# Kernel optimization log

Measured on AMD Instinct MI355X. Metric: run time of the kernel, lower is better.

## Reference

```python
import jax, jax.numpy as jnp
import numpy as np

T, IN_DIM, HID, OUT = 32768, 500, 300, 100


def setup_inputs() -> dict:
    key = jax.random.key(0)
    ks = jax.random.split(key, 12)
    s_in = 1.0 / np.sqrt(HID)
    inp = {
        'input_seq': jax.random.normal(ks[0], (T, IN_DIM), jnp.float32),
        'W_ih0': jax.random.uniform(ks[1], (HID, IN_DIM), jnp.float32, -s_in, s_in),
        'W_hh0': jax.random.uniform(ks[2], (HID, HID), jnp.float32, -s_in, s_in),
        'b_ih0': jax.random.uniform(ks[3], (HID,), jnp.float32, -s_in, s_in),
        'b_hh0': jax.random.uniform(ks[4], (HID,), jnp.float32, -s_in, s_in),
        'W_ih1': jax.random.uniform(ks[5], (HID, HID), jnp.float32, -s_in, s_in),
        'W_hh1': jax.random.uniform(ks[6], (HID, HID), jnp.float32, -s_in, s_in),
        'b_ih1': jax.random.uniform(ks[7], (HID,), jnp.float32, -s_in, s_in),
        'b_hh1': jax.random.uniform(ks[8], (HID,), jnp.float32, -s_in, s_in),
        'W_lin': jax.random.uniform(ks[9], (OUT, HID), jnp.float32, -s_in, s_in),
        'b_lin': jax.random.uniform(ks[10], (OUT,), jnp.float32, -s_in, s_in),
    }
    return inp


def _rnn_layer(x_proj, W_hh):
    # x_proj: [T, H] = precomputed input projection + both biases
    # h_t = tanh(x_proj_t + h_{t-1} @ W_hh^T), h_0 = 0 (PyTorch nn.RNN semantics)
    def step(h, xp):
        h_new = jnp.tanh(xp + h @ W_hh.T)
        return h_new, h_new
    h0 = jnp.zeros((W_hh.shape[0],), x_proj.dtype)
    _, hs = jax.lax.scan(step, h0, x_proj)
    return hs  # [T, H]


def reference(input_seq, W_ih0, W_hh0, b_ih0, b_hh0, W_ih1, W_hh1, b_ih1, b_hh1, W_lin, b_lin):
    # Layer 0: batch-1 vanilla tanh RNN; vectorize input GEMM over all timesteps
    x0 = input_seq @ W_ih0.T + (b_ih0 + b_hh0)  # [T, HID]
    h0 = _rnn_layer(x0, W_hh0)
    # Layer 1 consumes layer-0 hidden sequence
    x1 = h0 @ W_ih1.T + (b_ih1 + b_hh1)  # [T, HID]
    h1 = _rnn_layer(x1, W_hh1)
    # Linear head over flattened [T, HID]
    return h1 @ W_lin.T + b_lin  # [T, OUT]
```

## Files before the change

### kernel.cpp

```cpp
#include <hip/hip_runtime.h>
#include <cstddef>

#define T_LEN 32768
#define HID   300
#define HP    304
#define HK    320
#define KC    10
#define IN_D  500
#define OUT_D 100
#define OUTP  104
#define DIST  8
#define CHUNK 64
#define NCHUNK (T_LEN / CHUNK)

typedef _Float16 f16x8 __attribute__((ext_vector_type(8)));
typedef float    f32x4 __attribute__((ext_vector_type(4)));

__device__ __align__(16) float    g_x  [(size_t)(T_LEN + DIST) * HP];
__device__ __align__(16) float    g_x1 [(size_t)(T_LEN + DIST) * HP];
__device__ __align__(16) _Float16 g_h0h[(size_t)T_LEN * HP];
__device__ __align__(16) float    g_h1 [(size_t)T_LEN * HP];
__device__ __align__(16) float    g_wt0[IN_D * HP];
__device__ __align__(16) float    g_wtl[HID * OUTP];
__device__ int g_flag0;
__device__ int g_flag1;

__global__ void k_reset() { g_flag0 = 0; g_flag1 = 0; }

__global__ void k_transpose(const float* __restrict__ src, int J, int K, int JP, int dst_sel)
{
    float* dst = (dst_sel == 0) ? g_wt0 : g_wtl;
    int idx = blockIdx.x * 256 + threadIdx.x;
    if (idx >= K * JP) return;
    int k = idx / JP, j = idx - k * JP;
    dst[idx] = (j < J) ? src[j * K + k] : 0.f;
}

__global__ __launch_bounds__(320) void k_gemm_in(const float* __restrict__ inp,
                                                 const float* __restrict__ b1,
                                                 const float* __restrict__ b2)
{
    __shared__ float lds[32 * IN_D];
    const int tid = threadIdx.x;
    const int t0  = blockIdx.x * 32;
    {
        const f32x4* src4 = (const f32x4*)(inp + (size_t)t0 * IN_D);
        f32x4* lds4 = (f32x4*)lds;
        const int n4 = (32 * IN_D) >> 2;
        for (int i = tid; i < n4; i += 320) lds4[i] = src4[i];
    }
    __syncthreads();
    const int j = tid;
    if (j >= HP) return;
    float acc[32];
#pragma unroll
    for (int i = 0; i < 32; i++) acc[i] = 0.f;
#pragma unroll 4
    for (int k = 0; k < IN_D; k++) {
        float w = g_wt0[k * HP + j];
#pragma unroll
        for (int i = 0; i < 32; i++) acc[i] += w * lds[i * IN_D + k];
    }
    const float bias = (j < HID) ? (b1[j] + b2[j]) : 0.f;
#pragma unroll 4
    for (int i = 0; i < 32; i++) g_x[(size_t)(t0 + i) * HP + j] = acc[i] + bias;
}

__global__ __launch_bounds__(128) void k_gemm_out(const float* __restrict__ blin,
                                                  float* __restrict__ out)
{
    __shared__ float lds[64 * HP];
    const int tid = threadIdx.x;
    const int t0  = blockIdx.x * 64;
    {
        const f32x4* src4 = (const f32x4*)(g_h1 + (size_t)t0 * HP);
        f32x4* lds4 = (f32x4*)lds;
        for (int i = tid; i < (64 * HP) >> 2; i += 128) lds4[i] = src4[i];
    }
    __syncthreads();
    const int j = tid;
    if (j >= OUTP) return;
    float acc[64];
#pragma unroll
    for (int i = 0; i < 64; i++) acc[i] = 0.f;
#pragma unroll 2
    for (int k = 0; k < HID; k++) {
        float w = g_wtl[k * OUTP + j];
#pragma unroll
        for (int i = 0; i < 64; i++) acc[i] += w * lds[i * HP + k];
    }
    if (j < OUT_D) {
        float b = blin[j];
        for (int i = 0; i < 64; i++) out[(size_t)(t0 + i) * OUT_D + j] = acc[i] + b;
    }
}

__device__ __forceinline__ float fast_tanh(float v)
{
    float e = __expf(2.f * v);
    return 1.f - 2.f * __builtin_amdgcn_rcpf(e + 1.f);
}

__device__ __forceinline__ float sel4(f32x4 a, bool c1, bool c2)
{
    float v01 = c1 ? a[1] : a[0];
    float v23 = c1 ? a[3] : a[2];
    return c2 ? v23 : v01;
}

__device__ __forceinline__ f16x8 loadw_frag(const float* __restrict__ W,
                                            int tile, int col, int g, int kc)
{
    const int row = tile * 16 + col;
    const int kb  = kc * 32 + g * 8;
    f16x8 f;
#pragma unroll
    for (int j = 0; j < 8; j++) {
        const int k = kb + j;
        float wv = (row < HID && k < HID) ? W[row * HID + k] : 0.f;
        f[j] = (_Float16)wv;
    }
    return f;
}

__device__ __forceinline__ void wait_flag(int* f, int target)
{
    if (threadIdx.x == 0) {
        while (__hip_atomic_load(f, __ATOMIC_ACQUIRE, __HIP_MEMORY_SCOPE_AGENT) < target)
            __builtin_amdgcn_s_sleep(8);
    }
    __syncthreads();
}

__device__ __forceinline__ void publish_flag(int* f, int v)
{
    __syncthreads();
    if (threadIdx.x == 0)
        __hip_atomic_store(f, v, __ATOMIC_RELEASE, __HIP_MEMORY_SCOPE_AGENT);
}

template<int ROLE0>
__device__ __forceinline__ void scan_role(_Float16 (*hlds)[HK],
                                          const float* __restrict__ Whh,
                                          const float* __restrict__ xin,
                                          _Float16* __restrict__ h16,
                                          float* __restrict__ h32)
{
    const int tid  = threadIdx.x;
    const int lane = tid & 63;
    const int wave = tid >> 6;
    const int col  = lane & 15;
    const int g    = lane >> 4;
    const int rr   = col & 3;
    const bool c1  = (col & 1) != 0;
    const bool c2  = (col & 2) != 0;
    const bool writer = (col < 4);

    const int tA = wave, tB = wave + 8, tC = wave + 16;
    const bool hasC = (wave < 3);
    const int rowA = tA * 16 + g * 4 + rr;
    const int rowB = tB * 16 + g * 4 + rr;
    const int rowC = tC * 16 + g * 4 + rr;

    for (int i = tid; i < 2 * HK; i += 512) ((_Float16*)hlds)[i] = (_Float16)0.f;

    f16x8 wA[KC], wB[KC], wC[KC];
#pragma unroll
    for (int kc = 0; kc < KC; kc++) {
        wA[kc] = loadw_frag(Whh, tA, col, g, kc);
        wB[kc] = loadw_frag(Whh, tB, col, g, kc);
        if (hasC) wC[kc] = loadw_frag(Whh, tC, col, g, kc);
        else {
            f16x8 z;
#pragma unroll
            for (int j = 0; j < 8; j++) z[j] = (_Float16)0.f;
            wC[kc] = z;
        }
    }

    __syncthreads();

    if (!ROLE0) wait_flag(&g_flag1, NCHUNK < 2 ? NCHUNK : 2);

    float xA[DIST], xB[DIST], xC[DIST];
#pragma unroll
    for (int s = 0; s < DIST; s++) {
        xA[s] = xin[(size_t)s * HP + rowA];
        xB[s] = xin[(size_t)s * HP + rowB];
        xC[s] = hasC ? xin[(size_t)s * HP + rowC] : 0.f;
    }

    const f32x4 Z = {0.f, 0.f, 0.f, 0.f};

#define STEP(t_, R_, s_) do {                                                          \
        float xvA = xA[s_], xvB = xB[s_], xvC = xC[s_];                                \
        xA[s_] = xin[(size_t)((t_) + DIST) * HP + rowA];                               \
        xB[s_] = xin[(size_t)((t_) + DIST) * HP + rowB];                               \
        if (hasC) xC[s_] = xin[(size_t)((t_) + DIST) * HP + rowC];                     \
        f16x8 bf[KC];                                                                  \
        _Pragma("unroll")                                                              \
        for (int kc = 0; kc < KC; kc++)                                                \
            bf[kc] = *(const f16x8*)&hlds[R_][kc * 32 + g * 8];                        \
        f32x4 aA0 = __builtin_amdgcn_mfma_f32_16x16x32_f16(wA[0], bf[0], Z, 0, 0, 0);  \
        f32x4 aB0 = __builtin_amdgcn_mfma_f32_16x16x32_f16(wB[0], bf[0], Z, 0, 0, 0);  \
        f32x4 aC0 = hasC ? __builtin_amdgcn_mfma_f32_16x16x32_f16(wC[0], bf[0], Z, 0, 0, 0) : Z; \
        f32x4 aA1 = __builtin_amdgcn_mfma_f32_16x16x32_f16(wA[5], bf[5], Z, 0, 0, 0);  \
        f32x4 aB1 = __builtin_amdgcn_mfma_f32_16x16x32_f16(wB[5], bf[5], Z, 0, 0, 0);  \
        f32x4 aC1 = hasC ? __builtin_amdgcn_mfma_f32_16x16x32_f16(wC[5], bf[5], Z, 0, 0, 0) : Z; \
        _Pragma("unroll")                                                              \
        for (int j = 1; j < 5; j++) {                                                  \
            aA0 = __builtin_amdgcn_mfma_f32_16x16x32_f16(wA[j], bf[j], aA0, 0, 0, 0);  \
            aB0 = __builtin_amdgcn_mfma_f32_16x16x32_f16(wB[j], bf[j], aB0, 0, 0, 0);  \
            if (hasC)                                                                  \
            aC0 = __builtin_amdgcn_mfma_f32_16x16x32_f16(wC[j], bf[j], aC0, 0, 0, 0);  \
            aA1 = __builtin_amdgcn_mfma_f32_16x16x32_f16(wA[j + 5], bf[j + 5], aA1, 0, 0, 0); \
            aB1 = __builtin_amdgcn_mfma_f32_16x16x32_f16(wB[j + 5], bf[j + 5], aB1, 0, 0, 0); \
            if (hasC)                                                                  \
            aC1 = __builtin_amdgcn_mfma_f32_16x16x32_f16(wC[j + 5], bf[j + 5], aC1, 0, 0, 0); \
        }                                                                              \
        float sA = sel4(aA0, c1, c2) + sel4(aA1, c1, c2);                              \
        float sB = sel4(aB0, c1, c2) + sel4(aB1, c1, c2);                              \
        float yA = fast_tanh(sA + xvA);                                                \
        float yB = fast_tanh(sB + xvB);                                                \
        float yC = 0.f;                                                                \
        if (hasC) {                                                                    \
            float sC = sel4(aC0, c1, c2) + sel4(aC1, c1, c2);                          \
            yC = fast_tanh(sC + xvC);                                                  \
        }                                                                              \
        if (writer) {                                                                  \
            _Float16 hA = (_Float16)yA, hB = (_Float16)yB, hC = (_Float16)yC;          \
            hlds[1 - (R_)][tA * 16 + g * 4 + col] = hA;                                \
            hlds[1 - (R_)][tB * 16 + g * 4 + col] = hB;                                \
            if (hasC) hlds[1 - (R_)][tC * 16 + g * 4 + col] = hC;                      \
            if (ROLE0) {                                                               \
                h16[(size_t)(t_) * HP + rowA] = hA;                                    \
                h16[(size_t)(t_) * HP + rowB] = hB;                                    \
                if (hasC) h16[(size_t)(t_) * HP + rowC] = hC;                          \
            } else {                                                                   \
                h32[(size_t)(t_) * HP + rowA] = yA;                                    \
                h32[(size_t)(t_) * HP + rowB] = yB;                                    \
                if (hasC) h32[(size_t)(t_) * HP + rowC] = yC;                          \
            }                                                                          \
        }                                                                              \
    } while (0)

#define BAR() asm volatile("s_waitcnt lgkmcnt(0)\n\ts_barrier" ::: "memory")

#pragma unroll 1
    for (int c = 0; c < NCHUNK; ++c) {
        if (!ROLE0 && c > 0) {
            int tgt = (c + 2) < NCHUNK ? (c + 2) : NCHUNK;
            wait_flag(&g_flag1, tgt);
        }
#pragma unroll 1
        for (int tt = 0; tt < CHUNK; tt += DIST) {
            const int tb = c * CHUNK + tt;
            STEP(tb + 0, 0, 0); BAR();
            STEP(tb + 1, 1, 1); BAR();
            STEP(tb + 2, 0, 2); BAR();
            STEP(tb + 3, 1, 3); BAR();
            STEP(tb + 4, 0, 4); BAR();
            STEP(tb + 5, 1, 5); BAR();
            STEP(tb + 6, 0, 6); BAR();
            STEP(tb + 7, 1, 7); BAR();
        }
        if (ROLE0) publish_flag(&g_flag0, c + 1);
    }
#undef STEP
#undef BAR
}

__device__ __forceinline__ void proj_role(const float* __restrict__ Wih,
                                          const float* __restrict__ b1,
                                          const float* __restrict__ b2)
{
    const int tid  = threadIdx.x;
    const int lane = tid & 63;
    const int wave = tid >> 6;
    const int col  = lane & 15;
    const int g    = lane >> 4;

    const int tA = wave, tB = wave + 8, tC = wave + 16;
    const bool hasC = (wave < 3);

    f16x8 wA[KC], wB[KC], wC[KC];
#pragma unroll
    for (int kc = 0; kc < KC; kc++) {
        wA[kc] = loadw_frag(Wih, tA, col, g, kc);
        wB[kc] = loadw_frag(Wih, tB, col, g, kc);
        if (hasC) wC[kc] = loadw_frag(Wih, tC, col, g, kc);
        else {
            f16x8 z;
#pragma unroll
            for (int j = 0; j < 8; j++) z[j] = (_Float16)0.f;
            wC[kc] = z;
        }
    }
    f32x4 bA, bB, bC;
#pragma unroll
    for (int e = 0; e < 4; e++) {
        int jA = tA * 16 + g * 4 + e, jB = tB * 16 + g * 4 + e, jC = tC * 16 + g * 4 + e;
        bA[e] = (jA < HID) ? b1[jA] + b2[jA] : 0.f;
        bB[e] = (jB < HID) ? b1[jB] + b2[jB] : 0.f;
        bC[e] = (hasC && jC < HID) ? b1[jC] + b2[jC] : 0.f;
    }

    const f32x4 zero4 = {0.f, 0.f, 0.f, 0.f};

#pragma unroll 1
    for (int c = 0; c < NCHUNK; ++c) {
        wait_flag(&g_flag0, c + 1);
        const int tbase = c * CHUNK;
#pragma unroll
        for (int tg = 0; tg < 4; ++tg) {
            const int t = tbase + tg * 16 + col;
            f16x8 bf[KC];
#pragma unroll
            for (int kc = 0; kc < KC; ++kc)
                bf[kc] = *(const f16x8*)&g_h0h[(size_t)t * HP + kc * 32 + g * 8];
            f32x4 aA = zero4, aB = zero4, aC = zero4;
#pragma unroll
            for (int kc = 0; kc < KC; ++kc) {
                aA = __builtin_amdgcn_mfma_f32_16x16x32_f16(wA[kc], bf[kc], aA, 0, 0, 0);
                aB = __builtin_amdgcn_mfma_f32_16x16x32_f16(wB[kc], bf[kc], aB, 0, 0, 0);
                if (hasC)
                aC = __builtin_amdgcn_mfma_f32_16x16x32_f16(wC[kc], bf[kc], aC, 0, 0, 0);
            }
            *(f32x4*)&g_x1[(size_t)t * HP + tA * 16 + g * 4] = aA + bA;
            *(f32x4*)&g_x1[(size_t)t * HP + tB * 16 + g * 4] = aB + bB;
            if (hasC)
            *(f32x4*)&g_x1[(size_t)t * HP + tC * 16 + g * 4] = aC + bC;
        }
        publish_flag(&g_flag1, c + 1);
    }
}

__global__ __launch_bounds__(512, 2) void k_pipeline(const float* __restrict__ W_hh0,
                                                     const float* __restrict__ W_ih1,
                                                     const float* __restrict__ b_ih1,
                                                     const float* __restrict__ b_hh1,
                                                     const float* __restrict__ W_hh1)
{
    __shared__ __align__(16) _Float16 hlds[2][HK];
    if (blockIdx.x == 0)
        scan_role<1>(hlds, W_hh0, g_x, g_h0h, nullptr);
    else if (blockIdx.x == 1)
        proj_role(W_ih1, b_ih1, b_hh1);
    else
        scan_role<0>(hlds, W_hh1, g_x1, nullptr, g_h1);
}

extern "C" void kernel_launch(void* const* d_in, const int* in_sizes, int n_in,
                              void* d_out, int out_size, void* d_ws, size_t ws_size,
                              hipStream_t stream)
{
    (void)in_sizes; (void)n_in; (void)d_ws; (void)ws_size; (void)out_size;
    const float* input = (const float*)d_in[0];
    const float* W_ih0 = (const float*)d_in[1];
    const float* W_hh0 = (const float*)d_in[2];
    const float* b_ih0 = (const float*)d_in[3];
    const float* b_hh0 = (const float*)d_in[4];
    const float* W_ih1 = (const float*)d_in[5];
    const float* W_hh1 = (const float*)d_in[6];
    const float* b_ih1 = (const float*)d_in[7];
    const float* b_hh1 = (const float*)d_in[8];
    const float* W_lin = (const float*)d_in[9];
    const float* b_lin = (const float*)d_in[10];
    float* out = (float*)d_out;

    k_reset<<<dim3(1), dim3(1), 0, stream>>>();
    k_transpose<<<dim3((IN_D * HP + 255) / 256), dim3(256), 0, stream>>>(W_ih0, HID, IN_D, HP, 0);
    k_transpose<<<dim3((HID * OUTP + 255) / 256), dim3(256), 0, stream>>>(W_lin, OUT_D, HID, OUTP, 2);

    k_gemm_in<<<dim3(T_LEN / 32), dim3(320), 0, stream>>>(input, b_ih0, b_hh0);

    k_pipeline<<<dim3(3), dim3(512), 0, stream>>>(W_hh0, W_ih1, b_ih1, b_hh1, W_hh1);

    k_gemm_out<<<dim3(T_LEN / 64), dim3(128), 0, stream>>>(b_lin, out);
}
```

Measured before the change: 24.42 ms.

## Fold x-projection into MFMA accumulator and split recurrence into four chains

The recurrent step now loads the input projection as a 4-wide vector and uses it as the starting accumulator of the first MFMA chain, removing the scalar add after the reduction. The 10 K-chunks are split across four independent accumulator chains instead of two, shortening the serial MFMA dependency on the per-timestep critical path. Layer-1 hidden states are stored in fp16 and widened in the output GEMM, which halves that traffic at some precision cost. The prefetch distance drops from 8 to 2 and the unroll shrinks, lowering register pressure but exposing more load latency.

```diff
diff --git a/kernel.cpp b/kernel.cpp
--- a/kernel.cpp
+++ b/kernel.cpp
@@ -9,17 +9,17 @@
 #define IN_D  500
 #define OUT_D 100
 #define OUTP  104
-#define DIST  8
+#define DIST  2
 #define CHUNK 64
 #define NCHUNK (T_LEN / CHUNK)
 
 typedef _Float16 f16x8 __attribute__((ext_vector_type(8)));
 typedef float    f32x4 __attribute__((ext_vector_type(4)));
 
-__device__ __align__(16) float    g_x  [(size_t)(T_LEN + DIST) * HP];
-__device__ __align__(16) float    g_x1 [(size_t)(T_LEN + DIST) * HP];
-__device__ __align__(16) _Float16 g_h0h[(size_t)T_LEN * HP];
-__device__ __align__(16) float    g_h1 [(size_t)T_LEN * HP];
+__device__ __align__(16) float    g_x  [(size_t)(T_LEN + 8) * HP];
+__device__ __align__(16) float    g_x1 [(size_t)(T_LEN + 8) * HP];
+__device__ __align__(16) _Float16 g_h0h[(size_t)T_LEN * HP + 64];
+__device__ __align__(16) _Float16 g_h1h[(size_t)T_LEN * HP + 64];
 __device__ __align__(16) float    g_wt0[IN_D * HP];
 __device__ __align__(16) float    g_wtl[HID * OUTP];
 __device__ int g_flag0;
@@ -73,9 +73,14 @@
     const int tid = threadIdx.x;
     const int t0  = blockIdx.x * 64;
     {
-        const f32x4* src4 = (const f32x4*)(g_h1 + (size_t)t0 * HP);
-        f32x4* lds4 = (f32x4*)lds;
-        for (int i = tid; i < (64 * HP) >> 2; i += 128) lds4[i] = src4[i];
+        const f16x8* src8 = (const f16x8*)(g_h1h + (size_t)t0 * HP);
+        const int n8 = (64 * HP) / 8;
+        for (int i = tid; i < n8; i += 128) {
+            f16x8 v = src8[i];
+            float* d = &lds[i * 8];
+#pragma unroll
+            for (int e = 0; e < 8; e++) d[e] = (float)v[e];
+        }
     }
     __syncthreads();
     const int j = tid;
@@ -139,28 +144,28 @@
         __hip_atomic_store(f, v, __ATOMIC_RELEASE, __HIP_MEMORY_SCOPE_AGENT);
 }
 
+#define MF(a_, b_, c_) __builtin_amdgcn_mfma_f32_16x16x32_f16((a_), (b_), (c_), 0, 0, 0)
+
 template<int ROLE0>
 __device__ __forceinline__ void scan_role(_Float16 (*hlds)[HK],
                                           const float* __restrict__ Whh,
                                           const float* __restrict__ xin,
-                                          _Float16* __restrict__ h16,
-                                          float* __restrict__ h32)
+                                          _Float16* __restrict__ hseq)
 {
     const int tid  = threadIdx.x;
     const int lane = tid & 63;
     const int wave = tid >> 6;
     const int col  = lane & 15;
     const int g    = lane >> 4;
-    const int rr   = col & 3;
     const bool c1  = (col & 1) != 0;
     const bool c2  = (col & 2) != 0;
     const bool writer = (col < 4);
 
     const int tA = wave, tB = wave + 8, tC = wave + 16;
     const bool hasC = (wave < 3);
-    const int rowA = tA * 16 + g * 4 + rr;
-    const int rowB = tB * 16 + g * 4 + rr;
-    const int rowC = tC * 16 + g * 4 + rr;
+    const int wbA = tA * 16 + g * 4;
+    const int wbB = tB * 16 + g * 4;
+    const int wbC = tC * 16 + g * 4;
 
     for (int i = tid; i < 2 * HK; i += 512) ((_Float16*)hlds)[i] = (_Float16)0.f;
 
@@ -182,65 +187,66 @@
 
     if (!ROLE0) wait_flag(&g_flag1, NCHUNK < 2 ? NCHUNK : 2);
 
-    float xA[DIST], xB[DIST], xC[DIST];
+    const f32x4 Z = {0.f, 0.f, 0.f, 0.f};
+
+    f32x4 xA[DIST], xB[DIST], xC[DIST];
 #pragma unroll
     for (int s = 0; s < DIST; s++) {
-        xA[s] = xin[(size_t)s * HP + rowA];
-        xB[s] = xin[(size_t)s * HP + rowB];
-        xC[s] = hasC ? xin[(size_t)s * HP + rowC] : 0.f;
-    }
-
-    const f32x4 Z = {0.f, 0.f, 0.f, 0.f};
+        xA[s] = *(const f32x4*)&xin[(size_t)s * HP + wbA];
+        xB[s] = *(const f32x4*)&xin[(size_t)s * HP + wbB];
+        xC[s] = hasC ? *(const f32x4*)&xin[(size_t)s * HP + wbC] : Z;
+    }
 
 #define STEP(t_, R_, s_) do {                                                          \
-        float xvA = xA[s_], xvB = xB[s_], xvC = xC[s_];                                \
-        xA[s_] = xin[(size_t)((t_) + DIST) * HP + rowA];                               \
-        xB[s_] = xin[(size_t)((t_) + DIST) * HP + rowB];                               \
-        if (hasC) xC[s_] = xin[(size_t)((t_) + DIST) * HP + rowC];                     \
         f16x8 bf[KC];                                                                  \
         _Pragma("unroll")                                                              \
         for (int kc = 0; kc < KC; kc++)                                                \
             bf[kc] = *(const f16x8*)&hlds[R_][kc * 32 + g * 8];                        \
-        f32x4 aA0 = __builtin_amdgcn_mfma_f32_16x16x32_f16(wA[0], bf[0], Z, 0, 0, 0);  \
-        f32x4 aB0 = __builtin_amdgcn_mfma_f32_16x16x32_f16(wB[0], bf[0], Z, 0, 0, 0);  \
-        f32x4 aC0 = hasC ? __builtin_amdgcn_mfma_f32_16x16x32_f16(wC[0], bf[0], Z, 0, 0, 0) : Z; \
-        f32x4 aA1 = __builtin_amdgcn_mfma_f32_16x16x32_f16(wA[5], bf[5], Z, 0, 0, 0);  \
-        f32x4 aB1 = __builtin_amdgcn_mfma_f32_16x16x32_f16(wB[5], bf[5], Z, 0, 0, 0);  \
-        f32x4 aC1 = hasC ? __builtin_amdgcn_mfma_f32_16x16x32_f16(wC[5], bf[5], Z, 0, 0, 0) : Z; \
-        _Pragma("unroll")                                                              \
-        for (int j = 1; j < 5; j++) {                                                  \
-            aA0 = __builtin_amdgcn_mfma_f32_16x16x32_f16(wA[j], bf[j], aA0, 0, 0, 0);  \
-            aB0 = __builtin_amdgcn_mfma_f32_16x16x32_f16(wB[j], bf[j], aB0, 0, 0, 0);  \
-            if (hasC)                                                                  \
-            aC0 = __builtin_amdgcn_mfma_f32_16x16x32_f16(wC[j], bf[j], aC0, 0, 0, 0);  \
-            aA1 = __builtin_amdgcn_mfma_f32_16x16x32_f16(wA[j + 5], bf[j + 5], aA1, 0, 0, 0); \
-            aB1 = __builtin_amdgcn_mfma_f32_16x16x32_f16(wB[j + 5], bf[j + 5], aB1, 0, 0, 0); \
-            if (hasC)                                                                  \
-            aC1 = __builtin_amdgcn_mfma_f32_16x16x32_f16(wC[j + 5], bf[j + 5], aC1, 0, 0, 0); \
-        }                                                                              \
-        float sA = sel4(aA0, c1, c2) + sel4(aA1, c1, c2);                              \
-        float sB = sel4(aB0, c1, c2) + sel4(aB1, c1, c2);                              \
-        float yA = fast_tanh(sA + xvA);                                                \
-        float yB = fast_tanh(sB + xvB);                                                \
+        f32x4 xvA = xA[s_], xvB = xB[s_], xvC = xC[s_];                                \
+        xA[s_] = *(const f32x4*)&xin[(size_t)((t_) + DIST) * HP + wbA];                \
+        xB[s_] = *(const f32x4*)&xin[(size_t)((t_) + DIST) * HP + wbB];                \
+        if (hasC) xC[s_] = *(const f32x4*)&xin[(size_t)((t_) + DIST) * HP + wbC];      \
+                                            \
+        f32x4 cA0 = MF(wA[0], bf[0], xvA), cB0 = MF(wB[0], bf[0], xvB);                \
+        f32x4 cC0 = hasC ? MF(wC[0], bf[0], xvC) : Z;                                  \
+        f32x4 cA1 = MF(wA[3], bf[3], Z),   cB1 = MF(wB[3], bf[3], Z);                  \
+        f32x4 cC1 = hasC ? MF(wC[3], bf[3], Z) : Z;                                    \
+        f32x4 cA2 = MF(wA[6], bf[6], Z),   cB2 = MF(wB[6], bf[6], Z);                  \
+        f32x4 cC2 = hasC ? MF(wC[6], bf[6], Z) : Z;                                    \
+        f32x4 cA3 = MF(wA[8], bf[8], Z),   cB3 = MF(wB[8], bf[8], Z);                  \
+        f32x4 cC3 = hasC ? MF(wC[8], bf[8], Z) : Z;                                    \
+                                                                          \
+        cA0 = MF(wA[1], bf[1], cA0); cB0 = MF(wB[1], bf[1], cB0);                      \
+        if (hasC) cC0 = MF(wC[1], bf[1], cC0);                                         \
+        cA1 = MF(wA[4], bf[4], cA1); cB1 = MF(wB[4], bf[4], cB1);                      \
+        if (hasC) cC1 = MF(wC[4], bf[4], cC1);                                         \
+        cA2 = MF(wA[7], bf[7], cA2); cB2 = MF(wB[7], bf[7], cB2);                      \
+        if (hasC) cC2 = MF(wC[7], bf[7], cC2);                                         \
+        cA3 = MF(wA[9], bf[9], cA3); cB3 = MF(wB[9], bf[9], cB3);                      \
+        if (hasC) cC3 = MF(wC[9], bf[9], cC3);                                         \
+                                                        \
+        cA0 = MF(wA[2], bf[2], cA0); cB0 = MF(wB[2], bf[2], cB0);                      \
+        if (hasC) cC0 = MF(wC[2], bf[2], cC0);                                         \
+        cA1 = MF(wA[5], bf[5], cA1); cB1 = MF(wB[5], bf[5], cB1);                      \
+        if (hasC) cC1 = MF(wC[5], bf[5], cC1);                                         \
+                                                              \
+        f32x4 sumA = (cA0 + cA1) + (cA2 + cA3);                                        \
+        f32x4 sumB = (cB0 + cB1) + (cB2 + cB3);                                        \
+        float yA = fast_tanh(sel4(sumA, c1, c2));                                      \
+        float yB = fast_tanh(sel4(sumB, c1, c2));                                      \
         float yC = 0.f;                                                                \
         if (hasC) {                                                                    \
-            float sC = sel4(aC0, c1, c2) + sel4(aC1, c1, c2);                          \
-            yC = fast_tanh(sC + xvC);                                                  \
+            f32x4 sumC = (cC0 + cC1) + (cC2 + cC3);                                    \
+            yC = fast_tanh(sel4(sumC, c1, c2));                                        \
         }                                                                              \
         if (writer) {                                                                  \
             _Float16 hA = (_Float16)yA, hB = (_Float16)yB, hC = (_Float16)yC;          \
-            hlds[1 - (R_)][tA * 16 + g * 4 + col] = hA;                                \
-            hlds[1 - (R_)][tB * 16 + g * 4 + col] = hB;                                \
-            if (hasC) hlds[1 - (R_)][tC * 16 + g * 4 + col] = hC;                      \
-            if (ROLE0) {                                                               \
-                h16[(size_t)(t_) * HP + rowA] = hA;                                    \
-                h16[(size_t)(t_) * HP + rowB] = hB;                                    \
-                if (hasC) h16[(size_t)(t_) * HP + rowC] = hC;                          \
-            } else {                                                                   \
-                h32[(size_t)(t_) * HP + rowA] = yA;                                    \
-                h32[(size_t)(t_) * HP + rowB] = yB;                                    \
-                if (hasC) h32[(size_t)(t_) * HP + rowC] = yC;                          \
-            }                                                                          \
+            hlds[1 - (R_)][wbA + col] = hA;                                            \
+            hlds[1 - (R_)][wbB + col] = hB;                                            \
+            if (hasC) hlds[1 - (R_)][wbC + col] = hC;                                  \
+            hseq[(size_t)(t_) * HP + wbA + col] = hA;                                  \
+            hseq[(size_t)(t_) * HP + wbB + col] = hB;                                  \
+            if (hasC) hseq[(size_t)(t_) * HP + wbC + col] = hC;                        \
         }                                                                              \
     } while (0)
 
@@ -253,16 +259,10 @@
             wait_flag(&g_flag1, tgt);
         }
 #pragma unroll 1
-        for (int tt = 0; tt < CHUNK; tt += DIST) {
+        for (int tt = 0; tt < CHUNK; tt += 2) {
             const int tb = c * CHUNK + tt;
             STEP(tb + 0, 0, 0); BAR();
             STEP(tb + 1, 1, 1); BAR();
-            STEP(tb + 2, 0, 2); BAR();
-            STEP(tb + 3, 1, 3); BAR();
-            STEP(tb + 4, 0, 4); BAR();
-            STEP(tb + 5, 1, 5); BAR();
-            STEP(tb + 6, 0, 6); BAR();
-            STEP(tb + 7, 1, 7); BAR();
         }
         if (ROLE0) publish_flag(&g_flag0, c + 1);
     }
@@ -321,10 +321,9 @@
             f32x4 aA = zero4, aB = zero4, aC = zero4;
 #pragma unroll
             for (int kc = 0; kc < KC; ++kc) {
-                aA = __builtin_amdgcn_mfma_f32_16x16x32_f16(wA[kc], bf[kc], aA, 0, 0, 0);
-                aB = __builtin_amdgcn_mfma_f32_16x16x32_f16(wB[kc], bf[kc], aB, 0, 0, 0);
-                if (hasC)
-                aC = __builtin_amdgcn_mfma_f32_16x16x32_f16(wC[kc], bf[kc], aC, 0, 0, 0);
+                aA = MF(wA[kc], bf[kc], aA);
+                aB = MF(wB[kc], bf[kc], aB);
+                if (hasC) aC = MF(wC[kc], bf[kc], aC);
             }
             *(f32x4*)&g_x1[(size_t)t * HP + tA * 16 + g * 4] = aA + bA;
             *(f32x4*)&g_x1[(size_t)t * HP + tB * 16 + g * 4] = aB + bB;
@@ -343,11 +342,11 @@
 {
     __shared__ __align__(16) _Float16 hlds[2][HK];
     if (blockIdx.x == 0)
-        scan_role<1>(hlds, W_hh0, g_x, g_h0h, nullptr);
+        scan_role<1>(hlds, W_hh0, g_x, g_h0h);
     else if (blockIdx.x == 1)
         proj_role(W_ih1, b_ih1, b_hh1);
     else
-        scan_role<0>(hlds, W_hh1, g_x1, nullptr, g_h1);
+        scan_role<0>(hlds, W_hh1, g_x1, g_h1h);
 }
 
 extern "C" void kernel_launch(void* const* d_in, const int* in_sizes, int n_in,
```

Measured after the change: 26.04 ms. 1.07x slower.
